# Performance work log

Measured on AMD Instinct MI355X. Metric: run time of the kernel, lower is better.

## Reference

```python
import jax, jax.numpy as jnp
import numpy as np

B, S, D, H, DFF, N_LAYERS, BLK = 4, 1024, 1024, 16, 4096, 4, 64
DH = D // H
LN_EPS = 1e-5


def setup_inputs() -> dict:
    key = jax.random.key(0)
    ks = jax.random.split(key, 13)
    s = 0.02
    L = N_LAYERS
    return {
        "x": jax.random.normal(ks[0], (B, S, D), jnp.float32),
        "in_proj_w": jax.random.normal(ks[1], (L, 3 * D, D), jnp.float32) * s,
        "in_proj_b": jnp.zeros((L, 3 * D), jnp.float32),
        "out_w": jax.random.normal(ks[2], (L, D, D), jnp.float32) * s,
        "out_b": jnp.zeros((L, D), jnp.float32),
        "ln1_w": jnp.ones((L, D), jnp.float32),
        "ln1_b": jnp.zeros((L, D), jnp.float32),
        "lin1_w": jax.random.normal(ks[3], (L, DFF, D), jnp.float32) * s,
        "lin1_b": jnp.zeros((L, DFF), jnp.float32),
        "lin2_w": jax.random.normal(ks[4], (L, D, DFF), jnp.float32) * s,
        "lin2_b": jnp.zeros((L, D), jnp.float32),
        "ln2_w": jnp.ones((L, D), jnp.float32),
        "ln2_b": jnp.zeros((L, D), jnp.float32),
    }


def _layer_norm(x, w, b):
    mu = jnp.mean(x, axis=-1, keepdims=True)
    var = jnp.mean(jnp.square(x - mu), axis=-1, keepdims=True)
    return (x - mu) * jax.lax.rsqrt(var + LN_EPS) * w + b


def _forward(x, in_proj_w, in_proj_b, out_w, out_b, ln1_w, ln1_b,
             lin1_w, lin1_b, lin2_w, lin2_b, ln2_w, ln2_b):
    # block-causal additive bias: token may attend to current and previous blocks
    blk = jnp.arange(S) // BLK
    bias = jnp.where(blk[:, None] >= blk[None, :], 0.0, -jnp.inf)  # [S,S]
    scale = 1.0 / np.sqrt(DH).astype(np.float32)

    for l in range(N_LAYERS):
        # --- self-attention (post-norm, PyTorch TransformerEncoderLayer default) ---
        qkv = x @ in_proj_w[l].T + in_proj_b[l]            # [B,S,3D]
        q, k, v = jnp.split(qkv, 3, axis=-1)
        q = q.reshape(B, S, H, DH).transpose(0, 2, 1, 3)   # [B,H,S,DH]
        k = k.reshape(B, S, H, DH).transpose(0, 2, 1, 3)
        v = v.reshape(B, S, H, DH).transpose(0, 2, 1, 3)
        scores = jnp.einsum('bhqd,bhkd->bhqk', q, k) * scale + bias
        attn = jax.nn.softmax(scores, axis=-1)
        o = jnp.einsum('bhqk,bhkd->bhqd', attn, v)
        o = o.transpose(0, 2, 1, 3).reshape(B, S, D)
        o = o @ out_w[l].T + out_b[l]
        x = _layer_norm(x + o, ln1_w[l], ln1_b[l])
        # --- feed-forward (relu) ---
        h = jax.nn.relu(x @ lin1_w[l].T + lin1_b[l]) @ lin2_w[l].T + lin2_b[l]
        x = _layer_norm(x + h, ln2_w[l], ln2_b[l])
    return x


def reference(x, in_proj_w, in_proj_b, out_w, out_b, ln1_w, ln1_b,
              lin1_w, lin1_b, lin2_w, lin2_b, ln2_w, ln2_b):
    return _forward(x, in_proj_w, in_proj_b, out_w, out_b, ln1_w, ln1_b,
                    lin1_w, lin1_b, lin2_w, lin2_b, ln2_w, ln2_b)
```

## Files before the change

kernel.cpp:

```cpp
#include <hip/hip_runtime.h>
#include <stdint.h>

typedef __bf16 bf16;
typedef __bf16 bf16x8 __attribute__((ext_vector_type(8)));
typedef __bf16 bf16x4 __attribute__((ext_vector_type(4)));
typedef float  f32x4  __attribute__((ext_vector_type(4)));

#define B_   4
#define S_   1024
#define D_   1024
#define H_   16
#define DH_  64
#define DFF_ 4096
#define NL_  4
#define M_   (B_*S_)

__device__ __forceinline__ void async_copy16(const void* g, void* l) {
  __builtin_amdgcn_global_load_lds(
      (const __attribute__((address_space(1))) char*)(uintptr_t)g,
      (__attribute__((address_space(3))) char*)(uintptr_t)l,
      16, 0, 0);
}

#define WAITV4 asm volatile("s_waitcnt vmcnt(4)" ::: "memory")
#define WAITV0 asm volatile("s_waitcnt vmcnt(0)" ::: "memory")
#define BAR()  { asm volatile("" ::: "memory"); __builtin_amdgcn_s_barrier(); \
                 asm volatile("" ::: "memory"); }

template<int RELU, int MODE, int QKV>
__global__ __launch_bounds__(512, 2) void gemm256_kernel(
    const bf16* __restrict__ A,
    const bf16* __restrict__ W,
    const float* __restrict__ bias,
    float* __restrict__ Cf,
    bf16*  __restrict__ Cb,
    bf16*  __restrict__ VtOut,
    int N, int Ktot, int Kc, int gx, int PN, int PM, int bpk)
{
  __shared__ __align__(16) bf16 As[2][2][256*32];
  __shared__ __align__(16) bf16 Bs[2][2][256*32];

  const int tid  = threadIdx.x;
  const int wave = tid >> 6;
  const int lane = tid & 63;
  const int wr = wave >> 2, wc = wave & 3;
  const int q4  = lane >> 4;
  const int l15 = lane & 15;

  const int Lg  = blockIdx.x;
  const int kz  = Lg / bpk;
  const int L   = Lg % bpk;
  const int xcd = L & 7;
  const int s   = L >> 3;
  const int Gn  = gx / PN;
  const int bn = ((xcd % Gn)*PN + (s % PN)) << 8;
  const int bm = ((xcd / Gn)*PM + (s / PN)) << 8;
  const int kstart = kz * Kc;

  const int r_loc = lane >> 2, c4 = lane & 3;
  const int sko = (c4 ^ ((r_loc >> 1) & 3)) << 3;
  const bf16* agp[2]; const bf16* wgp[2];
#pragma unroll
  for (int j = 0; j < 2; ++j) {
    const int rr = j*128 + wave*16 + r_loc;
    agp[j] = A + (size_t)(bm + rr)*Ktot + kstart + sko;
    wgp[j] = W + (size_t)(bn + rr)*Ktot + kstart + sko;
  }

  auto stageA = [&](int buf, int kk, int koff) {
#pragma unroll
    for (int j = 0; j < 2; ++j)
      async_copy16(agp[j] + koff + kk*32, &As[buf][kk][(j*128 + wave*16)*32]);
  };
  auto stageB = [&](int buf, int kk, int koff) {
#pragma unroll
    for (int j = 0; j < 2; ++j)
      async_copy16(wgp[j] + koff + kk*32, &Bs[buf][kk][(j*128 + wave*16)*32]);
  };

  const int ch = ((q4 ^ ((l15 >> 1) & 3)) << 3);

  f32x4 acc[8][4] = {};
  const int steps = Kc / 64;

  stageA(0, 0, 0); stageB(0, 0, 0); stageA(0, 1, 0); stageB(0, 1, 0);
  WAITV4;
  BAR();

  int koff = 64;
  for (int t = 0; t < steps; ++t) {
    const int c = t & 1;
    const bool pf = (t + 1 < steps);
    bf16x8 bfr[4];
#pragma unroll
    for (int p = 0; p < 4; ++p) {
      const int kk = p >> 1, rh = p & 1;
      if (rh == 0) {
#pragma unroll
        for (int cf = 0; cf < 4; ++cf)
          bfr[cf] = *(const bf16x8*)&Bs[c][kk][(wc*64 + cf*16 + l15)*32 + ch];
      }
      bf16x8 af[4];
#pragma unroll
      for (int r4 = 0; r4 < 4; ++r4)
        af[r4] = *(const bf16x8*)&As[c][kk][(wr*128 + (rh*4 + r4)*16 + l15)*32 + ch];
      if (pf) {
        if      (p == 0) stageA(c ^ 1, 0, koff);
        else if (p == 1) stageB(c ^ 1, 0, koff);
        else if (p == 2) stageA(c ^ 1, 1, koff);
        else             stageB(c ^ 1, 1, koff);
      }
      BAR();
      __builtin_amdgcn_s_setprio(1);
#pragma unroll
      for (int r4 = 0; r4 < 4; ++r4)
#pragma unroll
        for (int cf = 0; cf < 4; ++cf)
          acc[rh*4 + r4][cf] = __builtin_amdgcn_mfma_f32_16x16x32_bf16(
              af[r4], bfr[cf], acc[rh*4 + r4][cf], 0, 0, 0);
      __builtin_amdgcn_s_setprio(0);
      if (p == 1) { if (pf) { WAITV4; } else { WAITV0; } }
      if (p == 3) { if (pf) { WAITV4; } }
      BAR();
    }
    koff += 64;
  }

  if (QKV && bn >= 2*D_) {
#pragma unroll
    for (int r = 0; r < 8; ++r) {
      const int row0 = bm + wr*128 + r*16 + q4*4;
      const int bidx = row0 >> 10, s0 = row0 & 1023;
#pragma unroll
      for (int cf = 0; cf < 4; ++cf) {
        const int col  = bn + wc*64 + cf*16 + l15;
        const int dcol = col - 2*D_;
        const int hh = dcol >> 6, dd = dcol & 63;
        const float bv = bias[col];
        bf16x4 pk;
#pragma unroll
        for (int i = 0; i < 4; ++i) pk[i] = (bf16)(acc[r][cf][i] + bv);
        *(bf16x4*)&VtOut[((size_t)((bidx*H_ + hh)*64 + dd))*S_ + s0] = pk;
      }
    }
  } else if (MODE == 2) {
    float* Cfz = Cf + (size_t)kz * ((size_t)M_ * N);
#pragma unroll
    for (int r = 0; r < 8; ++r) {
      const int row0 = bm + wr*128 + r*16 + q4*4;
#pragma unroll
      for (int cf = 0; cf < 4; ++cf) {
        const int col = bn + wc*64 + cf*16 + l15;
#pragma unroll
        for (int i = 0; i < 4; ++i)
          Cfz[(size_t)(row0 + i)*N + col] = acc[r][cf][i];
      }
    }
  } else {
#pragma unroll
    for (int r = 0; r < 8; ++r) {
      const int row0 = bm + wr*128 + r*16 + q4*4;
#pragma unroll
      for (int cf = 0; cf < 4; ++cf) {
        const int col = bn + wc*64 + cf*16 + l15;
        const float bv = bias[col];
#pragma unroll
        for (int i = 0; i < 4; ++i) {
          float v = acc[r][cf][i] + bv;
          if (RELU) v = fmaxf(v, 0.f);
          Cb[(size_t)(row0 + i)*N + col] = (bf16)v;
        }
      }
    }
  }
}

template<int RELU, int MODE, int QKV, int BK>
__global__ __launch_bounds__(256) void gemm_bt_kernel(
    const bf16* __restrict__ A, const bf16* __restrict__ W,
    const float* __restrict__ bias, float* __restrict__ Cf,
    bf16*  __restrict__ Cb, bf16*  __restrict__ VtOut,
    int N, int Ktot, int Kc, int gx, int PN, int PM, int bpk)
{
  constexpr int NI = (BK == 64) ? 4 : 2;
  __shared__ bf16 As[2][128*BK];
  __shared__ bf16 Bs[2][128*BK];

  const int tid  = threadIdx.x;
  const int wave = tid >> 6;
  const int lane = tid & 63;
  const int wr = wave >> 1, wc = wave & 1;
  const int q4  = lane >> 4;
  const int l15 = lane & 15;

  const int Lg  = blockIdx.x;
  const int kz  = Lg / bpk;
  const int L   = Lg % bpk;
  const int xcd = L & 7;
  const int s   = L >> 3;
  const int Gn  = gx / PN;
  const int bn = ((xcd % Gn)*PN + (s % PN)) << 7;
  const int bm = ((xcd / Gn)*PM + (s / PN)) << 7;
  const int kstart = kz * Kc;

  const bf16* agp[NI]; const bf16* wgp[NI];
  int ldsb[NI];
  if constexpr (BK == 64) {
    const int r_loc = lane >> 3, c8 = lane & 7;
#pragma unroll
    for (int j = 0; j < NI; ++j) {
      const int rr = wave*32 + j*8 + r_loc;
      const int ko = ((c8 ^ (rr & 7)) << 3);
      agp[j] = A + (size_t)(bm + rr)*Ktot + kstart + ko;
      wgp[j] = W + (size_t)(bn + rr)*Ktot + kstart + ko;
      ldsb[j] = (wave*32 + j*8) * 64;
    }
  } else {
    const int r_loc = lane >> 2, c4 = lane & 3;
#pragma unroll
    for (int j = 0; j < NI; ++j) {
      const int rr = wave*32 + j*16 + r_loc;
      const int ko = ((c4 ^ ((rr >> 1) & 3)) << 3);
      agp[j] = A + (size_t)(bm + rr)*Ktot + kstart + ko;
      wgp[j] = W + (size_t)(bn + rr)*Ktot + kstart + ko;
      ldsb[j] = (wave*32 + j*16) * 32;
    }
  }

  f32x4 acc[4][4] = {};
  const int steps = Kc / BK;

  auto stage = [&](int buf) {
#pragma unroll
    for (int j = 0; j < NI; ++j) {
      async_copy16(agp[j], &As[buf][ldsb[j]]);
      async_copy16(wgp[j], &Bs[buf][ldsb[j]]);
      agp[j] += BK; wgp[j] += BK;
    }
  };

  const int sl32 = (l15 >> 1) & 3;
  const int sl64 = l15 & 7;

  auto compute = [&](int buf) {
    if constexpr (BK == 64) {
#pragma unroll
      for (int kk = 0; kk < 2; ++kk) {
        const int ch = (((kk << 2) | q4) ^ sl64) << 3;
        bf16x8 af[4], bfr[4];
#pragma unroll
        for (int rf = 0; rf < 4; ++rf)
          af[rf] = *(const bf16x8*)&As[buf][(wr*64 + rf*16 + l15)*64 + ch];
#pragma unroll
        for (int cf = 0; cf < 4; ++cf)
          bfr[cf] = *(const bf16x8*)&Bs[buf][(wc*64 + cf*16 + l15)*64 + ch];
#pragma unroll
        for (int rf = 0; rf < 4; ++rf)
#pragma unroll
          for (int cf = 0; cf < 4; ++cf)
            acc[rf][cf] = __builtin_amdgcn_mfma_f32_16x16x32_bf16(
                af[rf], bfr[cf], acc[rf][cf], 0, 0, 0);
      }
    } else {
      const int ch = (q4 ^ sl32) << 3;
      bf16x8 af[4], bfr[4];
#pragma unroll
      for (int rf = 0; rf < 4; ++rf)
        af[rf] = *(const bf16x8*)&As[buf][(wr*64 + rf*16 + l15)*32 + ch];
#pragma unroll
      for (int cf = 0; cf < 4; ++cf)
        bfr[cf] = *(const bf16x8*)&Bs[buf][(wc*64 + cf*16 + l15)*32 + ch];
#pragma unroll
      for (int rf = 0; rf < 4; ++rf)
#pragma unroll
        for (int cf = 0; cf < 4; ++cf)
          acc[rf][cf] = __builtin_amdgcn_mfma_f32_16x16x32_bf16(
              af[rf], bfr[cf], acc[rf][cf], 0, 0, 0);
    }
  };

  stage(0);
  __syncthreads();
  for (int k = 0; k < steps; ++k) {
    const int cur = k & 1;
    if (k + 1 < steps) stage(cur ^ 1);
    compute(cur);
    __syncthreads();
  }

  if (QKV && bn >= 2*D_) {
#pragma unroll
    for (int r = 0; r < 4; ++r) {
      const int row0 = bm + wr*64 + r*16 + q4*4;
      const int bidx = row0 >> 10, s0 = row0 & 1023;
#pragma unroll
      for (int c = 0; c < 4; ++c) {
        const int col  = bn + wc*64 + c*16 + l15;
        const int dcol = col - 2*D_;
        const int hh = dcol >> 6, dd = dcol & 63;
        const float bv = bias[col];
        bf16x4 pk;
#pragma unroll
        for (int i = 0; i < 4; ++i) pk[i] = (bf16)(acc[r][c][i] + bv);
        *(bf16x4*)&VtOut[((size_t)((bidx*H_ + hh)*64 + dd))*S_ + s0] = pk;
      }
    }
  } else if (MODE == 2) {
    float* Cfz = Cf + (size_t)kz * ((size_t)M_ * N);
#pragma unroll
    for (int r = 0; r < 4; ++r) {
      const int row0 = bm + wr*64 + r*16 + q4*4;
#pragma unroll
      for (int c = 0; c < 4; ++c) {
        const int col = bn + wc*64 + c*16 + l15;
#pragma unroll
        for (int i = 0; i < 4; ++i)
          Cfz[(size_t)(row0 + i)*N + col] = acc[r][c][i];
      }
    }
  } else {
#pragma unroll
    for (int r = 0; r < 4; ++r) {
      const int row0 = bm + wr*64 + r*16 + q4*4;
#pragma unroll
      for (int c = 0; c < 4; ++c) {
        const int col = bn + wc*64 + c*16 + l15;
        const float bv = bias[c ? col : col];
#pragma unroll
        for (int i = 0; i < 4; ++i) {
          float v = acc[r][c][i] + bv;
          if (RELU) v = fmaxf(v, 0.f);
          Cb[(size_t)(row0 + i)*N + col] = (bf16)v;
        }
      }
    }
  }
}

__global__ __launch_bounds__(256) void attn_kernel(
    const bf16* __restrict__ qkv,
    const bf16* __restrict__ vt,
    bf16* __restrict__ out)
{
  const int L    = blockIdx.x;
  const int xcd  = L & 7, slot = L >> 3;
  const int qb0  = slot & 7;
  const int bh   = xcd*8 + (slot >> 3);
  const int b    = bh >> 4, h = bh & 15;
  const int tid  = threadIdx.x;
  const int wave = tid >> 6, lane = tid & 63;
  const int q4 = lane >> 4, l15 = lane & 15;
  const int r_loc = lane >> 3, c8 = lane & 7;

  __shared__ bf16 Ks[2][64*64];
  __shared__ bf16 Vs[2][64*64];
  __shared__ bf16 Ps[4][16*64];

  const size_t RS = 3*(size_t)D_;
  const bf16* kg = qkv + (size_t)(b*S_)*RS + D_ + h*64;
  const bf16* vg = vt + (size_t)bh*64*S_;

#define STAGE_KV(KT, BUF)                                              \
  {                                                                    \
    _Pragma("unroll")                                                  \
    for (int j = 0; j < 2; ++j) {                                      \
      const int rr = wave*16 + j*8 + r_loc;                            \
      const int ko = ((c8 ^ (rr & 7)) << 3);                           \
      async_copy16(kg + (size_t)((KT)*64 + rr)*RS + ko,                \
                   &Ks[BUF][(wave*16 + j*8)*64]);                      \
      async_copy16(vg + (size_t)rr*S_ + (KT)*64 + ko,                  \
                   &Vs[BUF][(wave*16 + j*8)*64]);                      \
    }                                                                  \
  }

  for (int pass = 0; pass < 2; ++pass) {
    const int qb = pass ? (15 - qb0) : qb0;
    const bf16* qg = qkv + (size_t)(b*S_ + qb*64)*RS + h*64;

    bf16x8 qf[2];
#pragma unroll
    for (int kk = 0; kk < 2; ++kk) {
      bf16x8 t = *(const bf16x8*)(qg + (size_t)(wave*16 + l15)*RS + kk*32 + (q4 << 3));
#pragma unroll
      for (int j = 0; j < 8; ++j) t[j] = (bf16)((float)t[j] * 0.125f);
      qf[kk] = t;
    }

    f32x4 o_acc[4] = {};
    float m_i = -1e30f, l_i = 0.f;

    STAGE_KV(0, 0)
    __syncthreads();

    for (int kt = 0; kt <= qb; ++kt) {
      const int cur = kt & 1;
      if (kt < qb) {
        if (cur) STAGE_KV(kt+1, 0) else STAGE_KV(kt+1, 1)
      }

      f32x4 sc[4] = {};
#pragma unroll
      for (int kk = 0; kk < 2; ++kk) {
        const int go = ((((kk << 2) | q4)) ^ (l15 & 7)) << 3;
#pragma unroll
        for (int m = 0; m < 4; ++m) {
          bf16x8 bk = *(const bf16x8*)&Ks[cur][(m*16 + l15)*64 + go];
          sc[m] = __builtin_amdgcn_mfma_f32_16x16x32_bf16(bk, qf[kk], sc[m], 0, 0, 0);
        }
      }

      float mx0 = fmaxf(fmaxf(sc[0][0], sc[0][1]), fmaxf(sc[0][2], sc[0][3]));
      float mx1 = fmaxf(fmaxf(sc[1][0], sc[1][1]), fmaxf(sc[1][2], sc[1][3]));
      float mx2 = fmaxf(fmaxf(sc[2][0], sc[2][1]), fmaxf(sc[2][2], sc[2][3]));
      float mx3 = fmaxf(fmaxf(sc[3][0], sc[3][1]), fmaxf(sc[3][2], sc[3][3]));
      float mx  = fmaxf(fmaxf(mx0, mx1), fmaxf(mx2, mx3));
      mx = fmaxf(mx, __shfl_xor(mx, 16, 64));
      mx = fmaxf(mx, __shfl_xor(mx, 32, 64));

      if (__any(mx > m_i + 8.f)) {
        const float m_new = fmaxf(m_i, mx);
        const float alpha = __expf(m_i - m_new);
        m_i = m_new;
        l_i *= alpha;
#pragma unroll
        for (int i = 0; i < 4; ++i) {
          const float av = __shfl(alpha, (lane & 48) | ((q4 << 2) | i), 64);
#pragma unroll
          for (int c = 0; c < 4; ++c) o_acc[c][i] *= av;
        }
      }

      float rs = 0.f;
#pragma unroll
      for (int m = 0; m < 4; ++m) {
        const float p0 = __expf(sc[m][0] - m_i);
        const float p1 = __expf(sc[m][1] - m_i);
        const float p2 = __expf(sc[m][2] - m_i);
        const float p3 = __expf(sc[m][3] - m_i);
        rs += (p0 + p1) + (p2 + p3);
        bf16x4 pk;
        pk[0] = (bf16)p0; pk[1] = (bf16)p1; pk[2] = (bf16)p2; pk[3] = (bf16)p3;
        const int cx = ((m << 2) | q4) ^ (l15 & 14);
        *(bf16x4*)&Ps[wave][(l15 << 6) | (cx << 2)] = pk;
      }
      rs += __shfl_xor(rs, 16, 64);
      rs += __shfl_xor(rs, 32, 64);
      l_i += rs;

#pragma unroll
      for (int kk = 0; kk < 2; ++kk) {
        const int pcx = (((kk << 3) | (q4 << 1)) ^ (l15 & 14));
        bf16x8 ap = *(const bf16x8*)&Ps[wave][(l15 << 6) | (pcx << 2)];
        const int go = ((((kk << 2) | q4)) ^ (l15 & 7)) << 3;
#pragma unroll
        for (int c = 0; c < 4; ++c) {
          bf16x8 bv = *(const bf16x8*)&Vs[cur][(c*16 + l15)*64 + go];
          o_acc[c] = __builtin_amdgcn_mfma_f32_16x16x32_bf16(ap, bv, o_acc[c], 0, 0, 0);
        }
      }
      __syncthreads();
    }

    bf16* obase = out + ((size_t)(b*S_ + qb*64 + wave*16))*D_ + h*64;
#pragma unroll
    for (int i = 0; i < 4; ++i) {
      const float li = __shfl(l_i, (lane & 48) | ((q4 << 2) | i), 64);
      const float inv = 1.f / li;
#pragma unroll
      for (int c = 0; c < 4; ++c)
        obase[(size_t)((q4 << 2) | i)*D_ + c*16 + l15] = (bf16)(o_acc[c][i] * inv);
    }
  }
#undef STAGE_KV
}

template<int NP>
__global__ __launch_bounds__(256) void add_ln_kernel(
    const float* __restrict__ xin, const float* __restrict__ parts,
    const float* __restrict__ ybias,
    const float* __restrict__ w, const float* __restrict__ bta,
    float* __restrict__ xout, bf16* __restrict__ xbf,
    float* __restrict__ extra)
{
  const int row = blockIdx.x;
  const int tid = threadIdx.x;
  const size_t base = (size_t)row * D_;
  const size_t PS = (size_t)M_ * D_;
  float v[4], sm = 0.f, ss = 0.f;
#pragma unroll
  for (int j = 0; j < 4; ++j) {
    int idx = tid + j*256;
    float y = ybias[idx];
#pragma unroll
    for (int pz = 0; pz < NP; ++pz) y += parts[(size_t)pz*PS + base + idx];
    v[j] = xin[base + idx] + y;
    sm += v[j]; ss += v[j]*v[j];
  }
#pragma unroll
  for (int off = 1; off < 64; off <<= 1) {
    sm += __shfl_xor(sm, off, 64);
    ss += __shfl_xor(ss, off, 64);
  }
  __shared__ float red[8];
  const int wave = tid >> 6, lane = tid & 63;
  if (lane == 0) { red[wave] = sm; red[4 + wave] = ss; }
  __syncthreads();
  sm = red[0] + red[1] + red[2] + red[3];
  ss = red[4] + red[5] + red[6] + red[7];
  const float mean = sm * (1.f/D_);
  const float var  = ss * (1.f/D_) - mean*mean;
  const float rstd = rsqrtf(var + 1e-5f);
#pragma unroll
  for (int j = 0; j < 4; ++j) {
    int idx = tid + j*256;
    float o = (v[j] - mean)*rstd*w[idx] + bta[idx];
    xout[base + idx] = o;
    xbf[base + idx]  = (bf16)o;
    if (extra) extra[base + idx] = o;
  }
}

__global__ __launch_bounds__(256) void conv_kernel(
    const float4* __restrict__ src, bf16x4* __restrict__ dst, int n4)
{
  int i = blockIdx.x*blockDim.x + threadIdx.x;
  const int stride = gridDim.x*blockDim.x;
  for (; i < n4; i += stride) {
    float4 f = src[i];
    bf16x4 o;
    o[0] = (bf16)f.x; o[1] = (bf16)f.y; o[2] = (bf16)f.z; o[3] = (bf16)f.w;
    dst[i] = o;
  }
}

__global__ __launch_bounds__(256) void init_x_kernel(
    const float4* __restrict__ src, float4* __restrict__ xf,
    bf16x4* __restrict__ xb, int n4)
{
  int i = blockIdx.x*blockDim.x + threadIdx.x;
  const int stride = gridDim.x*blockDim.x;
  for (; i < n4; i += stride) {
    float4 f = src[i];
    xf[i] = f;
    bf16x4 o;
    o[0] = (bf16)f.x; o[1] = (bf16)f.y; o[2] = (bf16)f.z; o[3] = (bf16)f.w;
    xb[i] = o;
  }
}

extern "C" void kernel_launch(void* const* d_in, const int* in_sizes, int n_in,
                              void* d_out, int out_size, void* d_ws, size_t ws_size,
                              hipStream_t stream) {
  const float* x    = (const float*)d_in[0];
  const float* inw  = (const float*)d_in[1];
  const float* inb  = (const float*)d_in[2];
  const float* outw = (const float*)d_in[3];
  const float* outb = (const float*)d_in[4];
  const float* ln1w = (const float*)d_in[5];
  const float* ln1b = (const float*)d_in[6];
  const float* l1w  = (const float*)d_in[7];
  const float* l1b  = (const float*)d_in[8];
  const float* l2w  = (const float*)d_in[9];
  const float* l2b  = (const float*)d_in[10];
  const float* ln2w = (const float*)d_in[11];
  const float* ln2b = (const float*)d_in[12];

  char* ws = (char*)d_ws;
  size_t off = 0;
  auto take = [&](size_t bytes) {
    char* p = ws + off;
    off = (off + bytes + 255) & ~(size_t)255;
    return p;
  };
  bf16*  w_in_bf  = (bf16*) take((size_t)NL_*3*D_*D_*2);
  bf16*  w_out_bf = (bf16*) take((size_t)NL_*D_*D_*2);
  bf16*  w_l1_bf  = (bf16*) take((size_t)NL_*DFF_*D_*2);
  bf16*  w_l2_bf  = (bf16*) take((size_t)NL_*D_*DFF_*2);
  float* x_f      = (float*)take((size_t)M_*D_*4);
  bf16*  x_b      = (bf16*) take((size_t)M_*D_*2);
  bf16*  qkv_b    = (bf16*) take((size_t)M_*3*D_*2);
  bf16*  vt_b     = (bf16*) take((size_t)B_*H_*DH_*S_*2);
  bf16*  at_b     = (bf16*) take((size_t)M_*D_*2);
  bf16*  h_b      = (bf16*) take((size_t)M_*DFF_*2);
  float* parts    = (float*)take((size_t)4*M_*D_*4);
  (void)ws_size; (void)in_sizes; (void)n_in;

  auto conv = [&](const float* s, bf16* d, size_t n) {
    int n4 = (int)(n >> 2);
    int grid = (n4 + 255) / 256; if (grid > 4096) grid = 4096;
    conv_kernel<<<grid, 256, 0, stream>>>((const float4*)s, (bf16x4*)d, n4);
  };
  conv(inw,  w_in_bf,  (size_t)NL_*3*D_*D_);
  conv(outw, w_out_bf, (size_t)NL_*D_*D_);
  conv(l1w,  w_l1_bf,  (size_t)NL_*DFF_*D_);
  conv(l2w,  w_l2_bf,  (size_t)NL_*D_*DFF_);
  init_x_kernel<<<4096, 256, 0, stream>>>((const float4*)x, (float4*)x_f,
                                          (bf16x4*)x_b, (int)((size_t)M_*D_ >> 2));

  for (int l = 0; l < NL_; ++l) {
    gemm256_kernel<0,1,1><<<192, 512, 0, stream>>>(
        x_b, w_in_bf + (size_t)l*3*D_*D_, inb + (size_t)l*3*D_,
        nullptr, qkv_b, vt_b, 3*D_, D_, D_, 12, 3, 8, 192);
    attn_kernel<<<512, 256, 0, stream>>>(qkv_b, vt_b, at_b);
    gemm_bt_kernel<0,2,0,64><<<512, 256, 0, stream>>>(
        at_b, w_out_bf + (size_t)l*D_*D_, nullptr,
        parts, nullptr, nullptr, D_, D_, D_/2, 8, 4, 8, 256);
    add_ln_kernel<2><<<M_, 256, 0, stream>>>(
        x_f, parts, outb + (size_t)l*D_,
        ln1w + (size_t)l*D_, ln1b + (size_t)l*D_, x_f, x_b, nullptr);
    gemm256_kernel<1,1,0><<<256, 512, 0, stream>>>(
        x_b, w_l1_bf + (size_t)l*DFF_*D_, l1b + (size_t)l*DFF_,
        nullptr, h_b, nullptr, DFF_, D_, D_, 16, 4, 8, 256);
    gemm256_kernel<0,2,0><<<256, 512, 0, stream>>>(
        h_b, w_l2_bf + (size_t)l*D_*DFF_, nullptr,
        parts, nullptr, nullptr, D_, DFF_, DFF_/4, 4, 1, 8, 64);
    add_ln_kernel<4><<<M_, 256, 0, stream>>>(
        x_f, parts, l2b + (size_t)l*D_,
        ln2w + (size_t)l*D_, ln2b + (size_t)l*D_, x_f, x_b,
        (l == NL_-1) ? (float*)d_out : nullptr);
  }
}
```

Baseline: 1.018 ms.

## Store split-K partials in bf16, vectorize add-LN, batch GEMM prefetch issue

The split-K partial sums from the out-projection and FFN2 GEMMs are now written as bf16 instead of fp32, which halves partial-buffer traffic in both the GEMM epilogues and the add+LayerNorm reduction. The add_ln kernel is rewritten to use float4 and bf16x4 vector loads and stores, with each thread handling four contiguous elements. In the 256-tile GEMM, the next-stage A and B loads are issued together in the first two phases rather than spread over four, and the wait counts are adjusted to match. Rounding partials to bf16 before summation costs accuracy, and issuing the prefetch earlier changes how loads overlap with compute.

```diff
diff --git a/kernel.cpp b/kernel.cpp
--- a/kernel.cpp
+++ b/kernel.cpp
@@ -22,6 +22,7 @@
       16, 0, 0);
 }
 
+#define WAITV8 asm volatile("s_waitcnt vmcnt(8)" ::: "memory")
 #define WAITV4 asm volatile("s_waitcnt vmcnt(4)" ::: "memory")
 #define WAITV0 asm volatile("s_waitcnt vmcnt(0)" ::: "memory")
 #define BAR()  { asm volatile("" ::: "memory"); __builtin_amdgcn_s_barrier(); \
@@ -32,7 +33,6 @@
     const bf16* __restrict__ A,
     const bf16* __restrict__ W,
     const float* __restrict__ bias,
-    float* __restrict__ Cf,
     bf16*  __restrict__ Cb,
     bf16*  __restrict__ VtOut,
     int N, int Ktot, int Kc, int gx, int PN, int PM, int bpk)
@@ -105,10 +105,8 @@
       for (int r4 = 0; r4 < 4; ++r4)
         af[r4] = *(const bf16x8*)&As[c][kk][(wr*128 + (rh*4 + r4)*16 + l15)*32 + ch];
       if (pf) {
-        if      (p == 0) stageA(c ^ 1, 0, koff);
-        else if (p == 1) stageB(c ^ 1, 0, koff);
-        else if (p == 2) stageA(c ^ 1, 1, koff);
-        else             stageB(c ^ 1, 1, koff);
+        if      (p == 0) { stageA(c ^ 1, 0, koff); stageB(c ^ 1, 0, koff); }
+        else if (p == 1) { stageA(c ^ 1, 1, koff); stageB(c ^ 1, 1, koff); }
       }
       BAR();
       __builtin_amdgcn_s_setprio(1);
@@ -119,7 +117,7 @@
           acc[rh*4 + r4][cf] = __builtin_amdgcn_mfma_f32_16x16x32_bf16(
               af[r4], bfr[cf], acc[rh*4 + r4][cf], 0, 0, 0);
       __builtin_amdgcn_s_setprio(0);
-      if (p == 1) { if (pf) { WAITV4; } else { WAITV0; } }
+      if (p == 1) { if (pf) { WAITV8; } else { WAITV0; } }
       if (p == 3) { if (pf) { WAITV4; } }
       BAR();
     }
@@ -144,7 +142,7 @@
       }
     }
   } else if (MODE == 2) {
-    float* Cfz = Cf + (size_t)kz * ((size_t)M_ * N);
+    bf16* Cpz = Cb + (size_t)kz * ((size_t)M_ * N);
 #pragma unroll
     for (int r = 0; r < 8; ++r) {
       const int row0 = bm + wr*128 + r*16 + q4*4;
@@ -153,7 +151,7 @@
         const int col = bn + wc*64 + cf*16 + l15;
 #pragma unroll
         for (int i = 0; i < 4; ++i)
-          Cfz[(size_t)(row0 + i)*N + col] = acc[r][cf][i];
+          Cpz[(size_t)(row0 + i)*N + col] = (bf16)acc[r][cf][i];
       }
     }
   } else {
@@ -175,11 +173,10 @@
   }
 }
 
-template<int RELU, int MODE, int QKV, int BK>
+template<int RELU, int MODE, int BK>
 __global__ __launch_bounds__(256) void gemm_bt_kernel(
     const bf16* __restrict__ A, const bf16* __restrict__ W,
-    const float* __restrict__ bias, float* __restrict__ Cf,
-    bf16*  __restrict__ Cb, bf16*  __restrict__ VtOut,
+    const float* __restrict__ bias, bf16* __restrict__ Cb,
     int N, int Ktot, int Kc, int gx, int PN, int PM, int bpk)
 {
   constexpr int NI = (BK == 64) ? 4 : 2;
@@ -288,44 +285,27 @@
     __syncthreads();
   }
 
-  if (QKV && bn >= 2*D_) {
+  if (MODE == 2) {
+    bf16* Cpz = Cb + (size_t)kz * ((size_t)M_ * N);
 #pragma unroll
     for (int r = 0; r < 4; ++r) {
       const int row0 = bm + wr*64 + r*16 + q4*4;
-      const int bidx = row0 >> 10, s0 = row0 & 1023;
 #pragma unroll
       for (int c = 0; c < 4; ++c) {
-        const int col  = bn + wc*64 + c*16 + l15;
-        const int dcol = col - 2*D_;
-        const int hh = dcol >> 6, dd = dcol & 63;
-        const float bv = bias[col];
-        bf16x4 pk;
-#pragma unroll
-        for (int i = 0; i < 4; ++i) pk[i] = (bf16)(acc[r][c][i] + bv);
-        *(bf16x4*)&VtOut[((size_t)((bidx*H_ + hh)*64 + dd))*S_ + s0] = pk;
-      }
-    }
-  } else if (MODE == 2) {
-    float* Cfz = Cf + (size_t)kz * ((size_t)M_ * N);
+        const int col = bn + wc*64 + c*16 + l15;
+#pragma unroll
+        for (int i = 0; i < 4; ++i)
+          Cpz[(size_t)(row0 + i)*N + col] = (bf16)acc[r][c][i];
+      }
+    }
+  } else {
 #pragma unroll
     for (int r = 0; r < 4; ++r) {
       const int row0 = bm + wr*64 + r*16 + q4*4;
 #pragma unroll
       for (int c = 0; c < 4; ++c) {
         const int col = bn + wc*64 + c*16 + l15;
-#pragma unroll
-        for (int i = 0; i < 4; ++i)
-          Cfz[(size_t)(row0 + i)*N + col] = acc[r][c][i];
-      }
-    }
-  } else {
-#pragma unroll
-    for (int r = 0; r < 4; ++r) {
-      const int row0 = bm + wr*64 + r*16 + q4*4;
-#pragma unroll
-      for (int c = 0; c < 4; ++c) {
-        const int col = bn + wc*64 + c*16 + l15;
-        const float bv = bias[c ? col : col];
+        const float bv = bias[col];
 #pragma unroll
         for (int i = 0; i < 4; ++i) {
           float v = acc[r][c][i] + bv;
@@ -476,7 +456,7 @@
 
 template<int NP>
 __global__ __launch_bounds__(256) void add_ln_kernel(
-    const float* __restrict__ xin, const float* __restrict__ parts,
+    const float* __restrict__ xin, const bf16* __restrict__ parts,
     const float* __restrict__ ybias,
     const float* __restrict__ w, const float* __restrict__ bta,
     float* __restrict__ xout, bf16* __restrict__ xbf,
@@ -486,16 +466,19 @@
   const int tid = threadIdx.x;
   const size_t base = (size_t)row * D_;
   const size_t PS = (size_t)M_ * D_;
-  float v[4], sm = 0.f, ss = 0.f;
-#pragma unroll
-  for (int j = 0; j < 4; ++j) {
-    int idx = tid + j*256;
-    float y = ybias[idx];
-#pragma unroll
-    for (int pz = 0; pz < NP; ++pz) y += parts[(size_t)pz*PS + base + idx];
-    v[j] = xin[base + idx] + y;
-    sm += v[j]; ss += v[j]*v[j];
-  }
+  const int i0 = tid << 2;
+
+  float4 xi = *(const float4*)&xin[base + i0];
+  float4 yb = *(const float4*)&ybias[i0];
+  float v[4] = { xi.x + yb.x, xi.y + yb.y, xi.z + yb.z, xi.w + yb.w };
+#pragma unroll
+  for (int pz = 0; pz < NP; ++pz) {
+    bf16x4 pk = *(const bf16x4*)&parts[(size_t)pz*PS + base + i0];
+#pragma unroll
+    for (int i = 0; i < 4; ++i) v[i] += (float)pk[i];
+  }
+  float sm = (v[0] + v[1]) + (v[2] + v[3]);
+  float ss = (v[0]*v[0] + v[1]*v[1]) + (v[2]*v[2] + v[3]*v[3]);
 #pragma unroll
   for (int off = 1; off < 64; off <<= 1) {
     sm += __shfl_xor(sm, off, 64);
@@ -510,14 +493,21 @@
   const float mean = sm * (1.f/D_);
   const float var  = ss * (1.f/D_) - mean*mean;
   const float rstd = rsqrtf(var + 1e-5f);
-#pragma unroll
-  for (int j = 0; j < 4; ++j) {
-    int idx = tid + j*256;
-    float o = (v[j] - mean)*rstd*w[idx] + bta[idx];
-    xout[base + idx] = o;
-    xbf[base + idx]  = (bf16)o;
-    if (extra) extra[base + idx] = o;
-  }
+
+  float4 wv = *(const float4*)&w[i0];
+  float4 bv = *(const float4*)&bta[i0];
+  float o[4];
+  o[0] = (v[0] - mean)*rstd*wv.x + bv.x;
+  o[1] = (v[1] - mean)*rstd*wv.y + bv.y;
+  o[2] = (v[2] - mean)*rstd*wv.z + bv.z;
+  o[3] = (v[3] - mean)*rstd*wv.w + bv.w;
+  float4 of = { o[0], o[1], o[2], o[3] };
+  *(float4*)&xout[base + i0] = of;
+  bf16x4 ob;
+#pragma unroll
+  for (int i = 0; i < 4; ++i) ob[i] = (bf16)o[i];
+  *(bf16x4*)&xbf[base + i0] = ob;
+  if (extra) *(float4*)&extra[base + i0] = of;
 }
 
 __global__ __launch_bounds__(256) void conv_kernel(
@@ -582,7 +572,7 @@
   bf16*  vt_b     = (bf16*) take((size_t)B_*H_*DH_*S_*2);
   bf16*  at_b     = (bf16*) take((size_t)M_*D_*2);
   bf16*  h_b      = (bf16*) take((size_t)M_*DFF_*2);
-  float* parts    = (float*)take((size_t)4*M_*D_*4);
+  bf16*  parts    = (bf16*) take((size_t)4*M_*D_*2);
   (void)ws_size; (void)in_sizes; (void)n_in;
 
   auto conv = [&](const float* s, bf16* d, size_t n) {
@@ -600,20 +590,20 @@
   for (int l = 0; l < NL_; ++l) {
     gemm256_kernel<0,1,1><<<192, 512, 0, stream>>>(
         x_b, w_in_bf + (size_t)l*3*D_*D_, inb + (size_t)l*3*D_,
-        nullptr, qkv_b, vt_b, 3*D_, D_, D_, 12, 3, 8, 192);
+        qkv_b, vt_b, 3*D_, D_, D_, 12, 3, 8, 192);
     attn_kernel<<<512, 256, 0, stream>>>(qkv_b, vt_b, at_b);
-    gemm_bt_kernel<0,2,0,64><<<512, 256, 0, stream>>>(
+    gemm_bt_kernel<0,2,64><<<512, 256, 0, stream>>>(
         at_b, w_out_bf + (size_t)l*D_*D_, nullptr,
-        parts, nullptr, nullptr, D_, D_, D_/2, 8, 4, 8, 256);
+        parts, D_, D_, D_/2, 8, 4, 8, 256);
     add_ln_kernel<2><<<M_, 256, 0, stream>>>(
         x_f, parts, outb + (size_t)l*D_,
         ln1w + (size_t)l*D_, ln1b + (size_t)l*D_, x_f, x_b, nullptr);
     gemm256_kernel<1,1,0><<<256, 512, 0, stream>>>(
         x_b, w_l1_bf + (size_t)l*DFF_*D_, l1b + (size_t)l*DFF_,
-        nullptr, h_b, nullptr, DFF_, D_, D_, 16, 4, 8, 256);
+        h_b, nullptr, DFF_, D_, D_, 16, 4, 8, 256);
     gemm256_kernel<0,2,0><<<256, 512, 0, stream>>>(
         h_b, w_l2_bf + (size_t)l*D_*DFF_, nullptr,
-        parts, nullptr, nullptr, D_, DFF_, DFF_/4, 4, 1, 8, 64);
+        parts, nullptr, D_, DFF_, DFF_/4, 4, 1, 8, 64);
     add_ln_kernel<4><<<M_, 256, 0, stream>>>(
         x_f, parts, l2b + (size_t)l*D_,
         ln2w + (size_t)l*D_, ln2b + (size_t)l*D_, x_f, x_b,
```

After: 1.032 ms. Within noise of the previous version (+1.4%).
